# Optimization experiments

Measured on AMD Instinct MI355X. Metric: run time of the kernel, lower is better.

The kernel has to match this reference:

```python
import jax, jax.numpy as jnp
import numpy as np

CODEC_RANGE = 1.0
COMMIT_WEIGHT = 0.1


def setup_inputs() -> dict:
    key = jax.random.key(0)
    ks = jax.random.split(key, 6)
    B, T, D, Dc, NQ, BINS = 8, 4096, 512, 256, 8, 1024
    return {
        "x": jax.random.normal(ks[0], (B, T, D), dtype=jnp.float32),
        "in_w": jax.random.normal(ks[1], (Dc, D), dtype=jnp.float32) * (1.0 / np.sqrt(D)),
        "in_b": jnp.zeros((Dc,), dtype=jnp.float32),
        "out_w": jax.random.normal(ks[2], (D, Dc), dtype=jnp.float32) * (1.0 / np.sqrt(Dc)),
        "out_b": jnp.zeros((D,), dtype=jnp.float32),
        "codebooks": jax.random.normal(ks[3], (NQ, BINS, Dc), dtype=jnp.float32),
    }


def reference(x, in_w, in_b, out_w, out_b, codebooks):
    # input projection + tanh range limiting
    h = jnp.tanh(x @ in_w.T + in_b) * CODEC_RANGE  # [B, T, Dc]

    def step(residual, codebook):
        # squared L2 distances: ||r||^2 - 2 r.e + ||e||^2  -> [B, T, bins]
        r2 = jnp.sum(residual * residual, axis=-1, keepdims=True)
        e2 = jnp.sum(codebook * codebook, axis=-1)  # [bins]
        dist = r2 - 2.0 * jnp.einsum("btd,nd->btn", residual, codebook) + e2
        idx = jnp.argmin(dist, axis=-1)  # [B, T]
        q = codebook[idx]  # gather -> [B, T, Dc]
        # commitment loss vs. detached quantized vectors
        commit = jnp.mean((jax.lax.stop_gradient(q) - residual) ** 2)
        return residual - q, (q, idx, commit)

    _, (qs, idxs, commits) = jax.lax.scan(step, h, codebooks)
    quantized = jnp.sum(qs, axis=0)  # [B, T, Dc]
    # straight-through estimator
    quantized = h + jax.lax.stop_gradient(quantized - h)
    out = quantized @ out_w.T + out_b  # [B, T, D]
    commit_loss = COMMIT_WEIGHT * jnp.sum(commits)
    return out, idxs, commit_loss
```

## Files before the change

kernel.cpp:

```cpp
#include <hip/hip_runtime.h>
#include <math.h>

#define DC 256
#define NBINS 1024
#define NQ 8
#define NTOK 32768
#define D_IN 512
#define DCH 32
#define TOK 64
#define STG_BLOCKS (NTOK / TOK)
#define MARGIN 5e-3f

typedef __attribute__((ext_vector_type(8))) short short8v;
typedef __attribute__((ext_vector_type(4))) float f32x4;

__device__ __forceinline__ unsigned short f2bf(float x) {
  unsigned u = __float_as_uint(x);
  return (unsigned short)((u + 0x7fffu + ((u >> 16) & 1u)) >> 16);
}
__device__ __forceinline__ float bf2f(unsigned short h) {
  return __uint_as_float(((unsigned)h) << 16);
}
__device__ __forceinline__ void store8s(unsigned short* dst, const unsigned short* v) {
  uint4 u;
  u.x = v[0] | ((unsigned)v[1] << 16); u.y = v[2] | ((unsigned)v[3] << 16);
  u.z = v[4] | ((unsigned)v[5] << 16); u.w = v[6] | ((unsigned)v[7] << 16);
  *reinterpret_cast<uint4*>(dst) = u;
}
__device__ __forceinline__ short8v pack8s(const unsigned short* v) {
  uint4 u;
  u.x = v[0] | ((unsigned)v[1] << 16); u.y = v[2] | ((unsigned)v[3] << 16);
  u.z = v[4] | ((unsigned)v[5] << 16); u.w = v[6] | ((unsigned)v[7] << 16);
  return __builtin_bit_cast(short8v, u);
}
__device__ __forceinline__ short8v load8s(const unsigned short* p) {
  return __builtin_bit_cast(short8v, *reinterpret_cast<const float4*>(p));
}

__device__ __forceinline__ float np_sumsq128(const float* a) {
#pragma clang fp contract(off)
  float r0 = a[0] * a[0], r1 = a[1] * a[1], r2 = a[2] * a[2], r3 = a[3] * a[3];
  float r4 = a[4] * a[4], r5 = a[5] * a[5], r6 = a[6] * a[6], r7 = a[7] * a[7];
  for (int i = 8; i < 128; i += 8) {
    r0 += a[i + 0] * a[i + 0]; r1 += a[i + 1] * a[i + 1];
    r2 += a[i + 2] * a[i + 2]; r3 += a[i + 3] * a[i + 3];
    r4 += a[i + 4] * a[i + 4]; r5 += a[i + 5] * a[i + 5];
    r6 += a[i + 6] * a[i + 6]; r7 += a[i + 7] * a[i + 7];
  }
  return ((r0 + r1) + (r2 + r3)) + ((r4 + r5) + (r6 + r7));
}
__device__ __forceinline__ float np_sumsq256(const float* a) {
#pragma clang fp contract(off)
  float lo = np_sumsq128(a);
  float hi = np_sumsq128(a + 128);
  return lo + hi;
}

__global__ void e2_np_kernel(const float* __restrict__ cb, float* __restrict__ e2) {
  int b = blockIdx.x * 256 + threadIdx.x;
  e2[b] = np_sumsq256(cb + (size_t)b * DC);
}

__global__ void presplit_kernel(const float* __restrict__ cb,
                                unsigned short* __restrict__ cb_h,
                                unsigned short* __restrict__ cb_l) {
  int id = blockIdx.x * 256 + threadIdx.x;
  int sk = id >> 10, bin = id & 1023;
  int s = sk >> 5, k8 = sk & 31;
  const float* src = cb + ((size_t)s * NBINS + bin) * DC + k8 * 8;
  unsigned short hh[8], ll[8];
#pragma unroll
  for (int j = 0; j < 8; ++j) {
    float x = src[j];
    unsigned short h = f2bf(x);
    hh[j] = h;
    ll[j] = f2bf(x - bf2f(h));
  }
  store8s(cb_h + (size_t)id * 8, hh);
  store8s(cb_l + (size_t)id * 8, ll);
}

__global__ __launch_bounds__(256, 4) void in_proj_kernel(
    const float* __restrict__ x, const float* __restrict__ in_w,
    const float* __restrict__ in_b, float* __restrict__ res) {
  __shared__ __align__(16) float aT[DCH][132];
  __shared__ __align__(16) float bT[DCH][68];
  const int thr = threadIdx.x;
  const int tx = thr & 15, ty = thr >> 4;
  const int m0 = blockIdx.x * 128, n0 = blockIdx.y * 64;
  float acc[8][4] = {};
  float s1[8][4] = {};
  for (int kc = 0; kc < D_IN; kc += DCH) {
    if (kc == 384) {
#pragma unroll
      for (int i = 0; i < 8; ++i)
#pragma unroll
        for (int j = 0; j < 4; ++j) { s1[i][j] = acc[i][j]; acc[i][j] = 0.f; }
    }
    __syncthreads();
#pragma unroll
    for (int i = 0; i < 4; ++i) {
      int q = thr + 256 * i;
      int m = q >> 3, kk = (q & 7) << 2;
      float4 v = *reinterpret_cast<const float4*>(x + (size_t)(m0 + m) * D_IN + kc + kk);
      aT[kk + 0][m] = v.x; aT[kk + 1][m] = v.y; aT[kk + 2][m] = v.z; aT[kk + 3][m] = v.w;
    }
#pragma unroll
    for (int i = 0; i < 2; ++i) {
      int q = thr + 256 * i;
      int m = q >> 3, kk = (q & 7) << 2;
      float4 w = *reinterpret_cast<const float4*>(in_w + (size_t)(n0 + m) * D_IN + kc + kk);
      bT[kk + 0][m] = w.x; bT[kk + 1][m] = w.y; bT[kk + 2][m] = w.z; bT[kk + 3][m] = w.w;
    }
    __syncthreads();
#pragma unroll 4
    for (int d = 0; d < DCH; ++d) {
      float4 a0 = *reinterpret_cast<const float4*>(&aT[d][ty * 8]);
      float4 a1 = *reinterpret_cast<const float4*>(&aT[d][ty * 8 + 4]);
      float4 b = *reinterpret_cast<const float4*>(&bT[d][tx * 4]);
      float av[8] = {a0.x, a0.y, a0.z, a0.w, a1.x, a1.y, a1.z, a1.w};
      float bv[4] = {b.x, b.y, b.z, b.w};
#pragma unroll
      for (int i = 0; i < 8; ++i)
#pragma unroll
        for (int j = 0; j < 4; ++j) acc[i][j] = fmaf(av[i], bv[j], acc[i][j]);
    }
  }
#pragma unroll
  for (int i = 0; i < 8; ++i) {
    int m = m0 + ty * 8 + i, n = n0 + tx * 4;
    float4 hv;
#pragma unroll
    for (int j = 0; j < 4; ++j) {
#pragma clang fp contract(off)
      float c = s1[i][j] + acc[i][j];
      float pre = c + in_b[n + j];
      ((float*)&hv)[j] = tanhf(pre);
    }
    *reinterpret_cast<float4*>(res + (size_t)m * DC + n) = hv;
  }
}

__global__ __launch_bounds__(256, 2) void score_kernel(
    const float* __restrict__ e2,
    const unsigned short* __restrict__ cb_h, const unsigned short* __restrict__ cb_l,
    const float* __restrict__ res, int* __restrict__ win_g, int* __restrict__ flag_g,
    int s) {
  __shared__ __align__(16) unsigned short a_hi[32 * TOK * 8];
  __shared__ __align__(16) unsigned short a_lo[32 * TOK * 8];
  __shared__ float m1s[4 * TOK], m2s[4 * TOK];
  __shared__ int   i1s[4 * TOK];

  const int thr = threadIdx.x;
  const int lane = thr & 63;
  const int w = thr >> 6;
  const int lg = lane >> 4;
  const int lc = lane & 15;
  const int m0 = blockIdx.x * TOK;
  const float* e2s = e2 + (size_t)s * NBINS;
  const unsigned short* bhp = cb_h + (size_t)s * (32 * 1024 * 8);
  const unsigned short* blp = cb_l + (size_t)s * (32 * 1024 * 8);

  {
    int row = thr >> 2, d0 = (thr & 3) << 6;
    const float* rrow = res + (size_t)(m0 + row) * DC + d0;
#pragma unroll
    for (int c = 0; c < 8; ++c) {
      float4 r0 = *reinterpret_cast<const float4*>(rrow + c * 8);
      float4 r1 = *reinterpret_cast<const float4*>(rrow + c * 8 + 4);
      float rv[8] = {r0.x, r0.y, r0.z, r0.w, r1.x, r1.y, r1.z, r1.w};
      unsigned short hh[8], ll[8];
#pragma unroll
      for (int j = 0; j < 8; ++j) {
        float xv = -2.0f * rv[j];
        unsigned short h = f2bf(xv);
        hh[j] = h; ll[j] = f2bf(xv - bf2f(h));
      }
      int k8 = (d0 >> 3) + c;
      store8s(a_hi + ((size_t)k8 * TOK + row) * 8, hh);
      store8s(a_lo + ((size_t)k8 * TOK + row) * 8, ll);
    }
  }
  m1s[thr] = 3.4028235e38f; m2s[thr] = 3.4028235e38f; i1s[thr] = 0;
  __syncthreads();

  for (int c = 0; c < 4; ++c) {
    const int bbase = w * 256 + c * 64;
    f32x4 acc[4][4];
#pragma unroll
    for (int nt = 0; nt < 4; ++nt) {
      float ev = e2s[bbase + nt * 16 + lc];
      f32x4 iv = {ev, ev, ev, ev};
#pragma unroll
      for (int rt = 0; rt < 4; ++rt) acc[rt][nt] = iv;
    }
#pragma unroll 2
    for (int kstep = 0; kstep < 8; ++kstep) {
      short8v ah[4], al[4];
#pragma unroll
      for (int rt = 0; rt < 4; ++rt) {
        int off = ((kstep * 4 + lg) * TOK + rt * 16 + lc) * 8;
        ah[rt] = load8s(a_hi + off);
        al[rt] = load8s(a_lo + off);
      }
      short8v bh[4], bl[4];
#pragma unroll
      for (int nt = 0; nt < 4; ++nt) {
        size_t boff = ((size_t)(kstep * 4 + lg) * 1024 + bbase + nt * 16 + lc) * 8;
        bh[nt] = load8s(bhp + boff);
        bl[nt] = load8s(blp + boff);
      }
      __builtin_amdgcn_s_setprio(1);
#pragma unroll
      for (int nt = 0; nt < 4; ++nt)
#pragma unroll
        for (int rt = 0; rt < 4; ++rt)
          acc[rt][nt] = __builtin_amdgcn_mfma_f32_16x16x32_bf16(ah[rt], bh[nt], acc[rt][nt], 0, 0, 0);
#pragma unroll
      for (int nt = 0; nt < 4; ++nt)
#pragma unroll
        for (int rt = 0; rt < 4; ++rt)
          acc[rt][nt] = __builtin_amdgcn_mfma_f32_16x16x32_bf16(ah[rt], bl[nt], acc[rt][nt], 0, 0, 0);
#pragma unroll
      for (int nt = 0; nt < 4; ++nt)
#pragma unroll
        for (int rt = 0; rt < 4; ++rt)
          acc[rt][nt] = __builtin_amdgcn_mfma_f32_16x16x32_bf16(al[rt], bh[nt], acc[rt][nt], 0, 0, 0);
      __builtin_amdgcn_s_setprio(0);
    }
#pragma unroll
    for (int rt = 0; rt < 4; ++rt)
#pragma unroll
      for (int reg = 0; reg < 4; ++reg) {
        float m1 = 3.4028235e38f, m2 = 3.4028235e38f; int i1 = 0;
#pragma unroll
        for (int nt = 0; nt < 4; ++nt) {
          float v = acc[rt][nt][reg];
          int b = bbase + nt * 16 + lc;
          if (v < m1) { m2 = m1; m1 = v; i1 = b; }
          else m2 = fminf(m2, v);
        }
#pragma unroll
        for (int msk = 1; msk < 16; msk <<= 1) {
          float om1 = __shfl_xor(m1, msk, 64);
          float om2 = __shfl_xor(m2, msk, 64);
          int   oi1 = __shfl_xor(i1, msk, 64);
          if (om1 < m1 || (om1 == m1 && oi1 < i1)) { m2 = fminf(m1, om2); m1 = om1; i1 = oi1; }
          else m2 = fminf(m2, om1);
        }
        if (lc == 0) {
          int sidx = w * TOK + rt * 16 + lg * 4 + reg;
          float pm1 = m1s[sidx], pm2 = m2s[sidx]; int pi1 = i1s[sidx];
          if (m1 < pm1 || (m1 == pm1 && i1 < pi1)) {
            m1s[sidx] = m1; m2s[sidx] = fminf(pm1, m2); i1s[sidx] = i1;
          } else {
            m2s[sidx] = fminf(pm2, m1);
          }
        }
      }
  }
  __syncthreads();
  if (thr < TOK) {
    float m1 = m1s[thr], m2 = m2s[thr]; int i1 = i1s[thr];
#pragma unroll
    for (int ww = 1; ww < 4; ++ww) {
      float om1 = m1s[ww * TOK + thr], om2 = m2s[ww * TOK + thr];
      int oi1 = i1s[ww * TOK + thr];
      if (om1 < m1 || (om1 == m1 && oi1 < i1)) { m2 = fminf(m1, om2); m1 = om1; i1 = oi1; }
      else m2 = fminf(m2, om1);
    }
    win_g[m0 + thr] = i1;
    flag_g[m0 + thr] = (m2 - m1 < MARGIN) ? 1 : 0;
  }
}

__global__ __launch_bounds__(256) void fix_kernel(
    const float* __restrict__ cb, const float* __restrict__ e2,
    const int* __restrict__ win_g, const int* __restrict__ flag_g,
    float* __restrict__ res, float* __restrict__ idx_f, double* __restrict__ partial,
    int s) {
  __shared__ int win_l[TOK], flag_l[TOK];
  __shared__ __align__(16) float rrow_s[256];
  __shared__ float redf[4];
  __shared__ int   redi[4];
  __shared__ double wsum[4];
  const int thr = threadIdx.x;
  const int lane = thr & 63;
  const int w = thr >> 6;
  const int m0 = blockIdx.x * TOK;
  const float* cbs = cb + (size_t)s * NBINS * DC;
  const float* e2s = e2 + (size_t)s * NBINS;
  double sqacc = 0.0;

  if (thr < TOK) { win_l[thr] = win_g[m0 + thr]; flag_l[thr] = flag_g[m0 + thr]; }
  __syncthreads();
  for (int row = 0; row < TOK; ++row) {
    if (!flag_l[row]) continue;
    if (thr < 64)
      reinterpret_cast<float4*>(rrow_s)[thr] =
          reinterpret_cast<const float4*>(res + (size_t)(m0 + row) * DC)[thr];
    __syncthreads();
    float r2 = np_sumsq256(rrow_s);
    float best = 3.4028235e38f; int bb = 0;
#pragma unroll
    for (int jj = 0; jj < 4; ++jj) {
      int b = thr * 4 + jj;
      const float4* e4 = reinterpret_cast<const float4*>(cbs + (size_t)b * DC);
      const float4* r4 = reinterpret_cast<const float4*>(rrow_s);
      float accv = 0.f;
      for (int q = 0; q < 64; ++q) {
        float4 ev = e4[q], rv = r4[q];
        accv = fmaf(rv.x, ev.x, accv);
        accv = fmaf(rv.y, ev.y, accv);
        accv = fmaf(rv.z, ev.z, accv);
        accv = fmaf(rv.w, ev.w, accv);
      }
      {
#pragma clang fp contract(off)
        float t = r2 - 2.0f * accv;
        float dist = t + e2s[b];
        if (dist < best) { best = dist; bb = b; }
      }
    }
#pragma unroll
    for (int msk = 1; msk < 64; msk <<= 1) {
      float ov = __shfl_xor(best, msk, 64);
      int   ob = __shfl_xor(bb, msk, 64);
      if (ov < best || (ov == best && ob < bb)) { best = ov; bb = ob; }
    }
    if (lane == 0) { redf[w] = best; redi[w] = bb; }
    __syncthreads();
    if (thr == 0) {
      float bs = redf[0]; int bfin = redi[0];
#pragma unroll
      for (int ww = 1; ww < 4; ++ww)
        if (redf[ww] < bs || (redf[ww] == bs && redi[ww] < bfin)) { bs = redf[ww]; bfin = redi[ww]; }
      win_l[row] = bfin;
    }
    __syncthreads();
  }
  {
    int row = thr >> 2, d0 = (thr & 3) << 6;
    int wbin = win_l[row];
    const float* erow = cbs + (size_t)wbin * DC + d0;
    float* rrow = res + (size_t)(m0 + row) * DC + d0;
#pragma unroll
    for (int c = 0; c < 8; ++c) {
      float4 r0 = *reinterpret_cast<const float4*>(rrow + c * 8);
      float4 r1 = *reinterpret_cast<const float4*>(rrow + c * 8 + 4);
      float4 e0 = *reinterpret_cast<const float4*>(erow + c * 8);
      float4 e1 = *reinterpret_cast<const float4*>(erow + c * 8 + 4);
      float nv[8] = {r0.x - e0.x, r0.y - e0.y, r0.z - e0.z, r0.w - e0.w,
                     r1.x - e1.x, r1.y - e1.y, r1.z - e1.z, r1.w - e1.w};
#pragma unroll
      for (int j = 0; j < 8; ++j) sqacc += (double)nv[j] * nv[j];
      *reinterpret_cast<float4*>(rrow + c * 8) = (float4){nv[0], nv[1], nv[2], nv[3]};
      *reinterpret_cast<float4*>(rrow + c * 8 + 4) = (float4){nv[4], nv[5], nv[6], nv[7]};
    }
    if (thr < TOK) idx_f[(size_t)s * NTOK + m0 + thr] = (float)win_l[thr];
  }
#pragma unroll
  for (int msk = 1; msk < 64; msk <<= 1) sqacc += __shfl_xor(sqacc, msk, 64);
  if (lane == 0) wsum[w] = sqacc;
  __syncthreads();
  if (thr == 0) {
    double t = 0.0;
#pragma unroll
    for (int ww = 0; ww < 4; ++ww) t += wsum[ww];
    partial[(size_t)s * STG_BLOCKS + blockIdx.x] = t;
  }
}

__global__ void finalize_kernel(const double* __restrict__ partial, float* __restrict__ out_last) {
  __shared__ double acc_s[64];
  int t = threadIdx.x;
  double a = 0.0;
  for (int i = 0; i < 64; ++i) a += partial[(size_t)t * 64 + i];
  acc_s[t] = a;
  __syncthreads();
  if (t == 0) {
    double tot = 0.0;
    for (int i = 0; i < 64; ++i) tot += acc_s[i];
    out_last[0] = (float)(0.1 * tot / 8388608.0);
  }
}

__global__ __launch_bounds__(256) void out_proj_kernel(
    const float* __restrict__ cb, const float* __restrict__ idx_f,
    const float* __restrict__ out_w, const float* __restrict__ out_b,
    float* __restrict__ out) {
  __shared__ __align__(16) unsigned short a_hi[32 * 32 * 8];
  __shared__ __align__(16) unsigned short a_lo[32 * 32 * 8];
  const int thr = threadIdx.x;
  const int lane = thr & 63;
  const int w = thr >> 6;
  const int lg = lane >> 4;
  const int lc = lane & 15;
  const int m0 = blockIdx.x * 32;

  {
    int row = thr >> 3, d0 = (thr & 7) << 5;
    int m = m0 + row;
    int idxs[NQ];
#pragma unroll
    for (int s = 0; s < NQ; ++s) idxs[s] = (int)idx_f[(size_t)s * NTOK + m];
#pragma unroll
    for (int c = 0; c < 4; ++c) {
      int d = d0 + c * 8;
      float q[8] = {0.f, 0.f, 0.f, 0.f, 0.f, 0.f, 0.f, 0.f};
#pragma unroll
      for (int s = 0; s < NQ; ++s) {
        const float4* e4 = reinterpret_cast<const float4*>(
            cb + ((size_t)s * NBINS + idxs[s]) * DC + d);
        float4 e0 = e4[0], e1 = e4[1];
        q[0] += e0.x; q[1] += e0.y; q[2] += e0.z; q[3] += e0.w;
        q[4] += e1.x; q[5] += e1.y; q[6] += e1.z; q[7] += e1.w;
      }
      unsigned short hh[8], ll[8];
#pragma unroll
      for (int j = 0; j < 8; ++j) {
        unsigned short h = f2bf(q[j]);
        hh[j] = h; ll[j] = f2bf(q[j] - bf2f(h));
      }
      int k8 = d >> 3;
      store8s(a_hi + ((size_t)k8 * 32 + row) * 8, hh);
      store8s(a_lo + ((size_t)k8 * 32 + row) * 8, ll);
    }
  }
  __syncthreads();

  f32x4 acc[2][8];
#pragma unroll
  for (int nt = 0; nt < 8; ++nt) {
    float bv = out_b[w * 128 + nt * 16 + lc];
    f32x4 iv = {bv, bv, bv, bv};
    acc[0][nt] = iv; acc[1][nt] = iv;
  }
#pragma unroll 2
  for (int kstep = 0; kstep < 8; ++kstep) {
    short8v ah[2], al[2];
#pragma unroll
    for (int rt = 0; rt < 2; ++rt) {
      int off = ((kstep * 4 + lg) * 32 + rt * 16 + lc) * 8;
      ah[rt] = load8s(a_hi + off);
      al[rt] = load8s(a_lo + off);
    }
#pragma unroll
    for (int nt = 0; nt < 8; ++nt) {
      int n = w * 128 + nt * 16 + lc;
      const float* wp = out_w + (size_t)n * DC + (kstep * 4 + lg) * 8;
      float4 w0 = *reinterpret_cast<const float4*>(wp);
      float4 w1 = *reinterpret_cast<const float4*>(wp + 4);
      float wv[8] = {w0.x, w0.y, w0.z, w0.w, w1.x, w1.y, w1.z, w1.w};
      unsigned short bhh[8], bll[8];
#pragma unroll
      for (int j = 0; j < 8; ++j) {
        unsigned short h = f2bf(wv[j]);
        bhh[j] = h; bll[j] = f2bf(wv[j] - bf2f(h));
      }
      short8v bh = pack8s(bhh), bl = pack8s(bll);
      acc[0][nt] = __builtin_amdgcn_mfma_f32_16x16x32_bf16(ah[0], bh, acc[0][nt], 0, 0, 0);
      acc[1][nt] = __builtin_amdgcn_mfma_f32_16x16x32_bf16(ah[1], bh, acc[1][nt], 0, 0, 0);
      acc[0][nt] = __builtin_amdgcn_mfma_f32_16x16x32_bf16(ah[0], bl, acc[0][nt], 0, 0, 0);
      acc[1][nt] = __builtin_amdgcn_mfma_f32_16x16x32_bf16(ah[1], bl, acc[1][nt], 0, 0, 0);
      acc[0][nt] = __builtin_amdgcn_mfma_f32_16x16x32_bf16(al[0], bh, acc[0][nt], 0, 0, 0);
      acc[1][nt] = __builtin_amdgcn_mfma_f32_16x16x32_bf16(al[1], bh, acc[1][nt], 0, 0, 0);
    }
  }
#pragma unroll
  for (int rt = 0; rt < 2; ++rt)
#pragma unroll
    for (int nt = 0; nt < 8; ++nt) {
      int n = w * 128 + nt * 16 + lc;
#pragma unroll
      for (int reg = 0; reg < 4; ++reg) {
        int m = m0 + rt * 16 + lg * 4 + reg;
        out[(size_t)m * D_IN + n] = acc[rt][nt][reg];
      }
    }
}

extern "C" void kernel_launch(void* const* d_in, const int* in_sizes, int n_in,
                              void* d_out, int out_size, void* d_ws, size_t ws_size,
                              hipStream_t stream) {
  (void)in_sizes; (void)n_in; (void)out_size; (void)d_ws; (void)ws_size;
  const float* x     = (const float*)d_in[0];
  const float* in_w  = (const float*)d_in[1];
  const float* in_b  = (const float*)d_in[2];
  const float* out_w = (const float*)d_in[3];
  const float* out_b = (const float*)d_in[4];
  const float* cb    = (const float*)d_in[5];
  float* out = (float*)d_out;
  float* res    = out;
  float* e2     = out + 8388608;
  double* part  = (double*)(out + 8404992);
  unsigned short* cb_h = (unsigned short*)(out + 9000000);
  unsigned short* cb_l = (unsigned short*)(out + 10500000);
  int* win_g   = (int*)(out + 11600000);
  int* flag_g  = (int*)(out + 11700000);
  float* idx_f  = out + 16777216;
  float* c_out  = out + 17039360;

  hipLaunchKernelGGL(e2_np_kernel, dim3(32), dim3(256), 0, stream, cb, e2);
  hipLaunchKernelGGL(presplit_kernel, dim3(1024), dim3(256), 0, stream, cb, cb_h, cb_l);
  hipLaunchKernelGGL(in_proj_kernel, dim3(256, 4), dim3(256), 0, stream, x, in_w, in_b, res);
  for (int s = 0; s < NQ; ++s) {
    hipLaunchKernelGGL(score_kernel, dim3(STG_BLOCKS), dim3(256), 0, stream,
                       e2, cb_h, cb_l, res, win_g, flag_g, s);
    hipLaunchKernelGGL(fix_kernel, dim3(STG_BLOCKS), dim3(256), 0, stream,
                       cb, e2, win_g, flag_g, res, idx_f, part, s);
  }
  hipLaunchKernelGGL(finalize_kernel, dim3(1), dim3(64), 0, stream, part, c_out);
  hipLaunchKernelGGL(out_proj_kernel, dim3(1024), dim3(256), 0, stream, cb, idx_f, out_w, out_b, out);
}
```

Before: 1.442 ms.

## Fuse per-stage fix with next-stage scoring and widen in_proj tile

The fix/rerank step of stage s now runs in the same kernel as the scoring of stage s+1. The updated residual is split into bf16 hi/lo straight into shared memory instead of being written to global and re-read by a separate score launch. This cuts the launch count from 16 to 9 and removes a global residual read per stage. In_proj also moves to a 128x128 tile with 8x8 per-thread accumulators and fewer blocks, which raises register pressure and lowers occupancy. The fused kernel uses more shared memory and does serial rerank work before the MFMA scoring.

```diff
diff --git a/kernel.cpp b/kernel.cpp
--- a/kernel.cpp
+++ b/kernel.cpp
@@ -80,22 +80,22 @@
   store8s(cb_l + (size_t)id * 8, ll);
 }
 
-__global__ __launch_bounds__(256, 4) void in_proj_kernel(
+__global__ __launch_bounds__(256, 2) void in_proj_kernel(
     const float* __restrict__ x, const float* __restrict__ in_w,
     const float* __restrict__ in_b, float* __restrict__ res) {
   __shared__ __align__(16) float aT[DCH][132];
-  __shared__ __align__(16) float bT[DCH][68];
+  __shared__ __align__(16) float bT[DCH][132];
   const int thr = threadIdx.x;
   const int tx = thr & 15, ty = thr >> 4;
-  const int m0 = blockIdx.x * 128, n0 = blockIdx.y * 64;
-  float acc[8][4] = {};
-  float s1[8][4] = {};
+  const int m0 = blockIdx.x * 128, n0 = blockIdx.y * 128;
+  float acc[8][8] = {};
+  float s1[8][8] = {};
   for (int kc = 0; kc < D_IN; kc += DCH) {
     if (kc == 384) {
 #pragma unroll
       for (int i = 0; i < 8; ++i)
 #pragma unroll
-        for (int j = 0; j < 4; ++j) { s1[i][j] = acc[i][j]; acc[i][j] = 0.f; }
+        for (int j = 0; j < 8; ++j) { s1[i][j] = acc[i][j]; acc[i][j] = 0.f; }
     }
     __syncthreads();
 #pragma unroll
@@ -106,84 +106,51 @@
       aT[kk + 0][m] = v.x; aT[kk + 1][m] = v.y; aT[kk + 2][m] = v.z; aT[kk + 3][m] = v.w;
     }
 #pragma unroll
-    for (int i = 0; i < 2; ++i) {
+    for (int i = 0; i < 4; ++i) {
       int q = thr + 256 * i;
       int m = q >> 3, kk = (q & 7) << 2;
       float4 w = *reinterpret_cast<const float4*>(in_w + (size_t)(n0 + m) * D_IN + kc + kk);
       bT[kk + 0][m] = w.x; bT[kk + 1][m] = w.y; bT[kk + 2][m] = w.z; bT[kk + 3][m] = w.w;
     }
     __syncthreads();
-#pragma unroll 4
+#pragma unroll 2
     for (int d = 0; d < DCH; ++d) {
       float4 a0 = *reinterpret_cast<const float4*>(&aT[d][ty * 8]);
       float4 a1 = *reinterpret_cast<const float4*>(&aT[d][ty * 8 + 4]);
-      float4 b = *reinterpret_cast<const float4*>(&bT[d][tx * 4]);
+      float4 b0 = *reinterpret_cast<const float4*>(&bT[d][tx * 8]);
+      float4 b1 = *reinterpret_cast<const float4*>(&bT[d][tx * 8 + 4]);
       float av[8] = {a0.x, a0.y, a0.z, a0.w, a1.x, a1.y, a1.z, a1.w};
-      float bv[4] = {b.x, b.y, b.z, b.w};
+      float bv[8] = {b0.x, b0.y, b0.z, b0.w, b1.x, b1.y, b1.z, b1.w};
 #pragma unroll
       for (int i = 0; i < 8; ++i)
 #pragma unroll
-        for (int j = 0; j < 4; ++j) acc[i][j] = fmaf(av[i], bv[j], acc[i][j]);
+        for (int j = 0; j < 8; ++j) acc[i][j] = fmaf(av[i], bv[j], acc[i][j]);
     }
   }
 #pragma unroll
   for (int i = 0; i < 8; ++i) {
-    int m = m0 + ty * 8 + i, n = n0 + tx * 4;
-    float4 hv;
-#pragma unroll
-    for (int j = 0; j < 4; ++j) {
+    int m = m0 + ty * 8 + i;
+#pragma unroll
+    for (int h = 0; h < 2; ++h) {
+      int n = n0 + tx * 8 + h * 4;
+      float4 hv;
+#pragma unroll
+      for (int j = 0; j < 4; ++j) {
 #pragma clang fp contract(off)
-      float c = s1[i][j] + acc[i][j];
-      float pre = c + in_b[n + j];
-      ((float*)&hv)[j] = tanhf(pre);
-    }
-    *reinterpret_cast<float4*>(res + (size_t)m * DC + n) = hv;
-  }
-}
-
-__global__ __launch_bounds__(256, 2) void score_kernel(
-    const float* __restrict__ e2,
-    const unsigned short* __restrict__ cb_h, const unsigned short* __restrict__ cb_l,
-    const float* __restrict__ res, int* __restrict__ win_g, int* __restrict__ flag_g,
-    int s) {
-  __shared__ __align__(16) unsigned short a_hi[32 * TOK * 8];
-  __shared__ __align__(16) unsigned short a_lo[32 * TOK * 8];
-  __shared__ float m1s[4 * TOK], m2s[4 * TOK];
-  __shared__ int   i1s[4 * TOK];
-
-  const int thr = threadIdx.x;
-  const int lane = thr & 63;
-  const int w = thr >> 6;
-  const int lg = lane >> 4;
-  const int lc = lane & 15;
-  const int m0 = blockIdx.x * TOK;
-  const float* e2s = e2 + (size_t)s * NBINS;
-  const unsigned short* bhp = cb_h + (size_t)s * (32 * 1024 * 8);
-  const unsigned short* blp = cb_l + (size_t)s * (32 * 1024 * 8);
-
-  {
-    int row = thr >> 2, d0 = (thr & 3) << 6;
-    const float* rrow = res + (size_t)(m0 + row) * DC + d0;
-#pragma unroll
-    for (int c = 0; c < 8; ++c) {
-      float4 r0 = *reinterpret_cast<const float4*>(rrow + c * 8);
-      float4 r1 = *reinterpret_cast<const float4*>(rrow + c * 8 + 4);
-      float rv[8] = {r0.x, r0.y, r0.z, r0.w, r1.x, r1.y, r1.z, r1.w};
-      unsigned short hh[8], ll[8];
-#pragma unroll
-      for (int j = 0; j < 8; ++j) {
-        float xv = -2.0f * rv[j];
-        unsigned short h = f2bf(xv);
-        hh[j] = h; ll[j] = f2bf(xv - bf2f(h));
-      }
-      int k8 = (d0 >> 3) + c;
-      store8s(a_hi + ((size_t)k8 * TOK + row) * 8, hh);
-      store8s(a_lo + ((size_t)k8 * TOK + row) * 8, ll);
-    }
-  }
-  m1s[thr] = 3.4028235e38f; m2s[thr] = 3.4028235e38f; i1s[thr] = 0;
-  __syncthreads();
-
+        float c = s1[i][h * 4 + j] + acc[i][h * 4 + j];
+        float pre = c + in_b[n + j];
+        ((float*)&hv)[j] = tanhf(pre);
+      }
+      *reinterpret_cast<float4*>(res + (size_t)m * DC + n) = hv;
+    }
+  }
+}
+
+__device__ __forceinline__ void score_phase(
+    const float* e2s, const unsigned short* bhp, const unsigned short* blp,
+    const unsigned short* a_hi, const unsigned short* a_lo,
+    float* m1s, float* m2s, int* i1s,
+    int* win_g, int* flag_g, int thr, int lane, int w, int lg, int lc, int m0) {
   for (int c = 0; c < 4; ++c) {
     const int bbase = w * 256 + c * 64;
     f32x4 acc[4][4];
@@ -272,6 +239,177 @@
     win_g[m0 + thr] = i1;
     flag_g[m0 + thr] = (m2 - m1 < MARGIN) ? 1 : 0;
   }
+}
+
+__device__ __forceinline__ void rerank_phase(
+    const float* cbs, const float* e2s, const float* res,
+    int* win_l, const int* flag_l, float* rrow_s, float* redf, int* redi,
+    int thr, int lane, int w, int m0) {
+  for (int row = 0; row < TOK; ++row) {
+    if (!flag_l[row]) continue;
+    if (thr < 64)
+      reinterpret_cast<float4*>(rrow_s)[thr] =
+          reinterpret_cast<const float4*>(res + (size_t)(m0 + row) * DC)[thr];
+    __syncthreads();
+    float r2 = np_sumsq256(rrow_s);
+    float best = 3.4028235e38f; int bb = 0;
+#pragma unroll
+    for (int jj = 0; jj < 4; ++jj) {
+      int b = thr * 4 + jj;
+      const float4* e4 = reinterpret_cast<const float4*>(cbs + (size_t)b * DC);
+      const float4* r4 = reinterpret_cast<const float4*>(rrow_s);
+      float accv = 0.f;
+      for (int q = 0; q < 64; ++q) {
+        float4 ev = e4[q], rv = r4[q];
+        accv = fmaf(rv.x, ev.x, accv);
+        accv = fmaf(rv.y, ev.y, accv);
+        accv = fmaf(rv.z, ev.z, accv);
+        accv = fmaf(rv.w, ev.w, accv);
+      }
+      {
+#pragma clang fp contract(off)
+        float t = r2 - 2.0f * accv;
+        float dist = t + e2s[b];
+        if (dist < best) { best = dist; bb = b; }
+      }
+    }
+#pragma unroll
+    for (int msk = 1; msk < 64; msk <<= 1) {
+      float ov = __shfl_xor(best, msk, 64);
+      int   ob = __shfl_xor(bb, msk, 64);
+      if (ov < best || (ov == best && ob < bb)) { best = ov; bb = ob; }
+    }
+    if (lane == 0) { redf[w] = best; redi[w] = bb; }
+    __syncthreads();
+    if (thr == 0) {
+      float bs = redf[0]; int bfin = redi[0];
+#pragma unroll
+      for (int ww = 1; ww < 4; ++ww)
+        if (redf[ww] < bs || (redf[ww] == bs && redi[ww] < bfin)) { bs = redf[ww]; bfin = redi[ww]; }
+      win_l[row] = bfin;
+    }
+    __syncthreads();
+  }
+}
+
+__global__ __launch_bounds__(256, 2) void score_kernel(
+    const float* __restrict__ e2,
+    const unsigned short* __restrict__ cb_h, const unsigned short* __restrict__ cb_l,
+    const float* __restrict__ res, int* __restrict__ win_g, int* __restrict__ flag_g,
+    int s) {
+  __shared__ __align__(16) unsigned short a_hi[32 * TOK * 8];
+  __shared__ __align__(16) unsigned short a_lo[32 * TOK * 8];
+  __shared__ float m1s[4 * TOK], m2s[4 * TOK];
+  __shared__ int   i1s[4 * TOK];
+  const int thr = threadIdx.x;
+  const int lane = thr & 63;
+  const int w = thr >> 6;
+  const int lg = lane >> 4;
+  const int lc = lane & 15;
+  const int m0 = blockIdx.x * TOK;
+  const float* e2s = e2 + (size_t)s * NBINS;
+  const unsigned short* bhp = cb_h + (size_t)s * (32 * 1024 * 8);
+  const unsigned short* blp = cb_l + (size_t)s * (32 * 1024 * 8);
+  {
+    int row = thr >> 2, d0 = (thr & 3) << 6;
+    const float* rrow = res + (size_t)(m0 + row) * DC + d0;
+#pragma unroll
+    for (int c = 0; c < 8; ++c) {
+      float4 r0 = *reinterpret_cast<const float4*>(rrow + c * 8);
+      float4 r1 = *reinterpret_cast<const float4*>(rrow + c * 8 + 4);
+      float rv[8] = {r0.x, r0.y, r0.z, r0.w, r1.x, r1.y, r1.z, r1.w};
+      unsigned short hh[8], ll[8];
+#pragma unroll
+      for (int j = 0; j < 8; ++j) {
+        float xv = -2.0f * rv[j];
+        unsigned short h = f2bf(xv);
+        hh[j] = h; ll[j] = f2bf(xv - bf2f(h));
+      }
+      int k8 = (d0 >> 3) + c;
+      store8s(a_hi + ((size_t)k8 * TOK + row) * 8, hh);
+      store8s(a_lo + ((size_t)k8 * TOK + row) * 8, ll);
+    }
+  }
+  m1s[thr] = 3.4028235e38f; m2s[thr] = 3.4028235e38f; i1s[thr] = 0;
+  __syncthreads();
+  score_phase(e2s, bhp, blp, a_hi, a_lo, m1s, m2s, i1s, win_g, flag_g,
+              thr, lane, w, lg, lc, m0);
+}
+
+__global__ __launch_bounds__(256, 2) void fixscore_kernel(
+    const float* __restrict__ cb, const float* __restrict__ e2,
+    const unsigned short* __restrict__ cb_h, const unsigned short* __restrict__ cb_l,
+    int* __restrict__ win_g, int* __restrict__ flag_g,
+    float* __restrict__ res, float* __restrict__ idx_f, double* __restrict__ partial,
+    int s) {
+  __shared__ __align__(16) unsigned short a_hi[32 * TOK * 8];
+  __shared__ __align__(16) unsigned short a_lo[32 * TOK * 8];
+  __shared__ float m1s[4 * TOK], m2s[4 * TOK];
+  __shared__ int   i1s[4 * TOK];
+  __shared__ int   win_l[TOK], flag_l[TOK];
+  __shared__ __align__(16) float rrow_s[256];
+  __shared__ float redf[4];
+  __shared__ int   redi[4];
+  __shared__ double wsum[4];
+  const int thr = threadIdx.x;
+  const int lane = thr & 63;
+  const int w = thr >> 6;
+  const int lg = lane >> 4;
+  const int lc = lane & 15;
+  const int m0 = blockIdx.x * TOK;
+  const float* cbs = cb + (size_t)s * NBINS * DC;
+  const float* e2s = e2 + (size_t)s * NBINS;
+  const float* e2n = e2 + (size_t)(s + 1) * NBINS;
+  const unsigned short* bhp = cb_h + (size_t)(s + 1) * (32 * 1024 * 8);
+  const unsigned short* blp = cb_l + (size_t)(s + 1) * (32 * 1024 * 8);
+  double sqacc = 0.0;
+
+  if (thr < TOK) { win_l[thr] = win_g[m0 + thr]; flag_l[thr] = flag_g[m0 + thr]; }
+  m1s[thr] = 3.4028235e38f; m2s[thr] = 3.4028235e38f; i1s[thr] = 0;
+  __syncthreads();
+  rerank_phase(cbs, e2s, res, win_l, flag_l, rrow_s, redf, redi, thr, lane, w, m0);
+  {
+    int row = thr >> 2, d0 = (thr & 3) << 6;
+    int wbin = win_l[row];
+    const float* erow = cbs + (size_t)wbin * DC + d0;
+    float* rrow = res + (size_t)(m0 + row) * DC + d0;
+#pragma unroll
+    for (int c = 0; c < 8; ++c) {
+      float4 r0 = *reinterpret_cast<const float4*>(rrow + c * 8);
+      float4 r1 = *reinterpret_cast<const float4*>(rrow + c * 8 + 4);
+      float4 e0 = *reinterpret_cast<const float4*>(erow + c * 8);
+      float4 e1 = *reinterpret_cast<const float4*>(erow + c * 8 + 4);
+      float nv[8] = {r0.x - e0.x, r0.y - e0.y, r0.z - e0.z, r0.w - e0.w,
+                     r1.x - e1.x, r1.y - e1.y, r1.z - e1.z, r1.w - e1.w};
+      unsigned short hh[8], ll[8];
+#pragma unroll
+      for (int j = 0; j < 8; ++j) {
+        sqacc += (double)nv[j] * nv[j];
+        float xv = -2.0f * nv[j];
+        unsigned short h = f2bf(xv);
+        hh[j] = h; ll[j] = f2bf(xv - bf2f(h));
+      }
+      *reinterpret_cast<float4*>(rrow + c * 8) = (float4){nv[0], nv[1], nv[2], nv[3]};
+      *reinterpret_cast<float4*>(rrow + c * 8 + 4) = (float4){nv[4], nv[5], nv[6], nv[7]};
+      int k8 = (d0 >> 3) + c;
+      store8s(a_hi + ((size_t)k8 * TOK + row) * 8, hh);
+      store8s(a_lo + ((size_t)k8 * TOK + row) * 8, ll);
+    }
+    if (thr < TOK) idx_f[(size_t)s * NTOK + m0 + thr] = (float)win_l[thr];
+  }
+#pragma unroll
+  for (int msk = 1; msk < 64; msk <<= 1) sqacc += __shfl_xor(sqacc, msk, 64);
+  if (lane == 0) wsum[w] = sqacc;
+  __syncthreads();
+  if (thr == 0) {
+    double t = 0.0;
+#pragma unroll
+    for (int ww = 0; ww < 4; ++ww) t += wsum[ww];
+    partial[(size_t)s * STG_BLOCKS + blockIdx.x] = t;
+  }
+  __syncthreads();
+  score_phase(e2n, bhp, blp, a_hi, a_lo, m1s, m2s, i1s, win_g, flag_g,
+              thr, lane, w, lg, lc, m0);
 }
 
 __global__ __launch_bounds__(256) void fix_kernel(
@@ -294,51 +432,7 @@
 
   if (thr < TOK) { win_l[thr] = win_g[m0 + thr]; flag_l[thr] = flag_g[m0 + thr]; }
   __syncthreads();
-  for (int row = 0; row < TOK; ++row) {
-    if (!flag_l[row]) continue;
-    if (thr < 64)
-      reinterpret_cast<float4*>(rrow_s)[thr] =
-          reinterpret_cast<const float4*>(res + (size_t)(m0 + row) * DC)[thr];
-    __syncthreads();
-    float r2 = np_sumsq256(rrow_s);
-    float best = 3.4028235e38f; int bb = 0;
-#pragma unroll
-    for (int jj = 0; jj < 4; ++jj) {
-      int b = thr * 4 + jj;
-      const float4* e4 = reinterpret_cast<const float4*>(cbs + (size_t)b * DC);
-      const float4* r4 = reinterpret_cast<const float4*>(rrow_s);
-      float accv = 0.f;
-      for (int q = 0; q < 64; ++q) {
-        float4 ev = e4[q], rv = r4[q];
-        accv = fmaf(rv.x, ev.x, accv);
-        accv = fmaf(rv.y, ev.y, accv);
-        accv = fmaf(rv.z, ev.z, accv);
-        accv = fmaf(rv.w, ev.w, accv);
-      }
-      {
-#pragma clang fp contract(off)
-        float t = r2 - 2.0f * accv;
-        float dist = t + e2s[b];
-        if (dist < best) { best = dist; bb = b; }
-      }
-    }
-#pragma unroll
-    for (int msk = 1; msk < 64; msk <<= 1) {
-      float ov = __shfl_xor(best, msk, 64);
-      int   ob = __shfl_xor(bb, msk, 64);
-      if (ov < best || (ov == best && ob < bb)) { best = ov; bb = ob; }
-    }
-    if (lane == 0) { redf[w] = best; redi[w] = bb; }
-    __syncthreads();
-    if (thr == 0) {
-      float bs = redf[0]; int bfin = redi[0];
-#pragma unroll
-      for (int ww = 1; ww < 4; ++ww)
-        if (redf[ww] < bs || (redf[ww] == bs && redi[ww] < bfin)) { bs = redf[ww]; bfin = redi[ww]; }
-      win_l[row] = bfin;
-    }
-    __syncthreads();
-  }
+  rerank_phase(cbs, e2s, res, win_l, flag_l, rrow_s, redf, redi, thr, lane, w, m0);
   {
     int row = thr >> 2, d0 = (thr & 3) << 6;
     int wbin = win_l[row];
@@ -397,7 +491,6 @@
   const int lg = lane >> 4;
   const int lc = lane & 15;
   const int m0 = blockIdx.x * 32;
-
   {
     int row = thr >> 3, d0 = (thr & 7) << 5;
     int m = m0 + row;
@@ -428,7 +521,6 @@
     }
   }
   __syncthreads();
-
   f32x4 acc[2][8];
 #pragma unroll
   for (int nt = 0; nt < 8; ++nt) {
@@ -503,13 +595,15 @@
 
   hipLaunchKernelGGL(e2_np_kernel, dim3(32), dim3(256), 0, stream, cb, e2);
   hipLaunchKernelGGL(presplit_kernel, dim3(1024), dim3(256), 0, stream, cb, cb_h, cb_l);
-  hipLaunchKernelGGL(in_proj_kernel, dim3(256, 4), dim3(256), 0, stream, x, in_w, in_b, res);
-  for (int s = 0; s < NQ; ++s) {
-    hipLaunchKernelGGL(score_kernel, dim3(STG_BLOCKS), dim3(256), 0, stream,
-                       e2, cb_h, cb_l, res, win_g, flag_g, s);
-    hipLaunchKernelGGL(fix_kernel, dim3(STG_BLOCKS), dim3(256), 0, stream,
-                       cb, e2, win_g, flag_g, res, idx_f, part, s);
-  }
+  hipLaunchKernelGGL(in_proj_kernel, dim3(256, 2), dim3(256), 0, stream, x, in_w, in_b, res);
+  hipLaunchKernelGGL(score_kernel, dim3(STG_BLOCKS), dim3(256), 0, stream,
+                     e2, cb_h, cb_l, res, win_g, flag_g, 0);
+  for (int s = 0; s < NQ - 1; ++s) {
+    hipLaunchKernelGGL(fixscore_kernel, dim3(STG_BLOCKS), dim3(256), 0, stream,
+                       cb, e2, cb_h, cb_l, win_g, flag_g, res, idx_f, part, s);
+  }
+  hipLaunchKernelGGL(fix_kernel, dim3(STG_BLOCKS), dim3(256), 0, stream,
+                     cb, e2, win_g, flag_g, res, idx_f, part, 7);
   hipLaunchKernelGGL(finalize_kernel, dim3(1), dim3(64), 0, stream, part, c_out);
   hipLaunchKernelGGL(out_proj_kernel, dim3(1024), dim3(256), 0, stream, cb, idx_f, out_w, out_b, out);
 }
```

New measurement: 1.479 ms. 1.03x slower.
